# Performance work log

Hardware: AMD Instinct MI355X
Metric: run time of the kernel (lower is better)

The kernel has to match this reference:

```python
import jax, jax.numpy as jnp
import numpy as np

D_MODEL = 1024
NHEAD = 16
D_K = D_MODEL // NHEAD


def setup_inputs() -> dict:
    key = jax.random.key(0)
    ks = jax.random.split(key, 12)
    B, L = 4, 2048
    s = 1.0 / np.sqrt(D_MODEL)
    inp = {
        "query": jax.random.normal(ks[0], (B, L, D_MODEL), jnp.float32),
        "key": jax.random.normal(ks[1], (B, L, D_MODEL), jnp.float32),
        "value": jax.random.normal(ks[2], (B, L, D_MODEL), jnp.float32),
        "Wq": jax.random.normal(ks[3], (D_MODEL, D_MODEL), jnp.float32) * s,
        "bq": jnp.zeros((D_MODEL,), jnp.float32),
        "Wk": jax.random.normal(ks[4], (D_MODEL, D_MODEL), jnp.float32) * s,
        "bk": jnp.zeros((D_MODEL,), jnp.float32),
        "Wv": jax.random.normal(ks[5], (D_MODEL, D_MODEL), jnp.float32) * s,
        "bv": jnp.zeros((D_MODEL,), jnp.float32),
        "Wo": jax.random.normal(ks[6], (D_MODEL, D_MODEL), jnp.float32) * s,
        "bo": jnp.zeros((D_MODEL,), jnp.float32),
    }
    return inp


def reference(query, key, value, Wq, bq, Wk, bk, Wv, bv, Wo, bo):
    B, Lq, _ = query.shape
    Lk = key.shape[1]
    # Linear projections, split into heads: [B, H, L, d_k]
    Q = (query @ Wq + bq).reshape(B, Lq, NHEAD, D_K).transpose(0, 2, 1, 3)
    K = (key @ Wk + bk).reshape(B, Lk, NHEAD, D_K).transpose(0, 2, 1, 3)
    V = (value @ Wv + bv).reshape(B, Lk, NHEAD, D_K).transpose(0, 2, 1, 3)
    scale = 1.0 / jnp.sqrt(jnp.asarray(D_K, Q.dtype))
    scores = jnp.einsum("bhqd,bhkd->bhqk", Q, K) * scale  # [B,H,Lq,Lk]
    attn = jax.nn.softmax(scores, axis=-1)
    context = jnp.einsum("bhqk,bhkd->bhqd", attn, V)
    context = context.transpose(0, 2, 1, 3).reshape(B, Lq, D_MODEL)
    return context @ Wo + bo
```

## Files before the change

kernel.cpp:

```cpp
#include <hip/hip_runtime.h>
#include <hip/hip_bf16.h>
#include <cstdint>
#include <cstddef>


typedef unsigned short u16;
typedef __bf16 bf8v __attribute__((ext_vector_type(8)));
typedef __bf16 bf4v __attribute__((ext_vector_type(4)));
typedef float f32x4 __attribute__((ext_vector_type(4)));

#define D_MODEL 1024
#define NHEAD   16
#define DK      64
#define BATCH   4
#define SEQ     2048
#define ROWS    (BATCH * SEQ)

__device__ __forceinline__ u16 f2b(float f) {
  union { float f; unsigned int i; } x; x.f = f;
  unsigned int r = x.i + 0x7fffu + ((x.i >> 16) & 1u);
  return (u16)(r >> 16);
}
__device__ __forceinline__ ushort4 pack4(float a, float b, float c, float d) {
  union { bf4v v; ushort4 u; } x;
  x.v[0] = (__bf16)a; x.v[1] = (__bf16)b; x.v[2] = (__bf16)c; x.v[3] = (__bf16)d;
  return x.u;
}
__device__ __forceinline__ bf8v cvt8(float4 a, float4 b) {
  bf8v r;
  r[0] = (__bf16)a.x; r[1] = (__bf16)a.y; r[2] = (__bf16)a.z; r[3] = (__bf16)a.w;
  r[4] = (__bf16)b.x; r[5] = (__bf16)b.y; r[6] = (__bf16)b.z; r[7] = (__bf16)b.w;
  return r;
}
__device__ __forceinline__ void async16(const void* g, void* l) {
  __builtin_amdgcn_global_load_lds((const __attribute__((address_space(1))) void*)g,
                                   (__attribute__((address_space(3))) void*)l, 16, 0, 0);
}
#define MFMA16(a, b, c) __builtin_amdgcn_mfma_f32_16x16x32_bf16(a, b, c, 0, 0, 0)

__global__ void wtrans_cvt_kernel(const float* __restrict__ w0, const float* __restrict__ w1,
                                  const float* __restrict__ w2, const float* __restrict__ w3,
                                  u16* __restrict__ dst4) {
  __shared__ float t[32][33];
  const float* src = (blockIdx.z == 0) ? w0 : (blockIdx.z == 1) ? w1
                   : (blockIdx.z == 2) ? w2 : w3;
  u16* dst = dst4 + (size_t)blockIdx.z * D_MODEL * D_MODEL;
  const int c0 = blockIdx.x * 32, r0 = blockIdx.y * 32;
  for (int i = threadIdx.y; i < 32; i += 8)
    t[i][threadIdx.x] = src[(size_t)(r0 + i) * D_MODEL + c0 + threadIdx.x];
  __syncthreads();
  for (int i = threadIdx.y; i < 32; i += 8)
    dst[(size_t)(c0 + i) * D_MODEL + r0 + threadIdx.x] = f2b(t[threadIdx.x][i]);
}

#define BM 128
#define BN 128
#define BK 32

__global__ __launch_bounds__(256) void gemm_qkv(
    const float* __restrict__ Aq, const float* __restrict__ Ak,
    const float* __restrict__ Av, const u16* __restrict__ wt,
    const float* __restrict__ bq, const float* __restrict__ bk,
    const float* __restrict__ bv, u16* __restrict__ Qw, u16* __restrict__ Kw,
    u16* __restrict__ Vt, float qscale) {
  __shared__ __align__(16) u16 As[BM * BK];
  __shared__ __align__(16) u16 Bs[BN * BK];
  const int z = blockIdx.y;
  const float* A = (z == 0) ? Aq : (z == 1) ? Ak : Av;
  const u16* Bt = wt + (size_t)z * D_MODEL * D_MODEL;
  const float* bias = (z == 0) ? bq : (z == 1) ? bk : bv;
  u16* out = (z == 0) ? Qw : (z == 1) ? Kw : Vt;
  const float oscale = (z == 0) ? qscale : 1.0f;

  const int lid = blockIdx.x;
  const int xcd = lid & 7, jj = lid >> 3;
  const int m0 = ((xcd << 3) + (jj >> 3)) * BM;
  const int n0 = (jj & 7) * BN;

  const int tid = threadIdx.x;
  const int lane = tid & 63, wave = tid >> 6;
  const int wm = wave >> 1, wn = wave & 1;
  const int quad = lane >> 4, l16 = lane & 15;
  const int K = 1024;

  f32x4 acc[4][4];
#pragma unroll
  for (int i = 0; i < 4; i++)
#pragma unroll
    for (int j = 0; j < 4; j++) acc[i][j] = (f32x4){0.f, 0.f, 0.f, 0.f};

  const int srow = tid >> 2;
  const int sch = ((tid & 3) ^ ((tid >> 3) & 3)) * 8;
  const int fsw = (quad ^ ((l16 >> 1) & 3)) * 8;
  const float* Ag0 = A + (size_t)(m0 + srow) * K + sch;
  const float* Ag1 = Ag0 + (size_t)64 * K;
  const u16* Bg = Bt + (size_t)(n0 + srow) * K + sch;

  float4 ar0 = *(const float4*)(Ag0);
  float4 ar1 = *(const float4*)(Ag0 + 4);
  float4 ar2 = *(const float4*)(Ag1);
  float4 ar3 = *(const float4*)(Ag1 + 4);

  for (int k0 = 0; k0 < K; k0 += BK) {
    async16(Bg + k0, &Bs[tid * 8]);
    async16(Bg + (size_t)64 * K + k0, &Bs[2048 + tid * 8]);
    *(bf8v*)&As[tid * 8]        = cvt8(ar0, ar1);
    *(bf8v*)&As[2048 + tid * 8] = cvt8(ar2, ar3);
    __syncthreads();
    if (k0 + BK < K) {
      ar0 = *(const float4*)(Ag0 + k0 + BK);
      ar1 = *(const float4*)(Ag0 + k0 + BK + 4);
      ar2 = *(const float4*)(Ag1 + k0 + BK);
      ar3 = *(const float4*)(Ag1 + k0 + BK + 4);
    }

    bf8v af[4], bfr[4];
#pragma unroll
    for (int i = 0; i < 4; i++)
      af[i] = *(const bf8v*)&As[(wm * 64 + i * 16 + l16) * BK + fsw];
#pragma unroll
    for (int j = 0; j < 4; j++)
      bfr[j] = *(const bf8v*)&Bs[(wn * 64 + j * 16 + l16) * BK + fsw];
    if (z < 2) {
#pragma unroll
      for (int i = 0; i < 4; i++)
#pragma unroll
        for (int j = 0; j < 4; j++)
          acc[i][j] = MFMA16(bfr[j], af[i], acc[i][j]);
    } else {
#pragma unroll
      for (int i = 0; i < 4; i++)
#pragma unroll
        for (int j = 0; j < 4; j++)
          acc[i][j] = MFMA16(af[i], bfr[j], acc[i][j]);
    }
    __syncthreads();
  }

  if (z < 2) {
#pragma unroll
    for (int i = 0; i < 4; i++) {
      const int m = m0 + wm * 64 + i * 16 + l16;
      const int b = m >> 11, l = m & 2047;
#pragma unroll
      for (int j = 0; j < 4; j++) {
        const int n = n0 + wn * 64 + j * 16 + quad * 4;
        const float4 bv4 = *(const float4*)&bias[n];
        const int h = n >> 6, d = n & 63;
        *(ushort4*)&out[(((size_t)(b * NHEAD + h) * SEQ + l) << 6) + d] =
            pack4((acc[i][j][0] + bv4.x) * oscale, (acc[i][j][1] + bv4.y) * oscale,
                  (acc[i][j][2] + bv4.z) * oscale, (acc[i][j][3] + bv4.w) * oscale);
      }
    }
  } else {
#pragma unroll
    for (int j = 0; j < 4; j++) {
      const int n = n0 + wn * 64 + j * 16 + l16;
      const float bvs = bias[n];
      const int h = n >> 6, d = n & 63;
#pragma unroll
      for (int i = 0; i < 4; i++) {
        const int row = m0 + wm * 64 + i * 16 + quad * 4;
        const int b = row >> 11, l = row & 2047;
        const int pl = (l & ~31) | ((l & 12) << 1) | ((l & 16) >> 2);
        *(ushort4*)&out[(((size_t)(b * NHEAD + h) * DK + d) << 11) + pl] =
            pack4(acc[i][j][0] + bvs, acc[i][j][1] + bvs,
                  acc[i][j][2] + bvs, acc[i][j][3] + bvs);
      }
    }
  }
}

__global__ __launch_bounds__(256) void gemm_out(const u16* __restrict__ A,
                                                const u16* __restrict__ Bt,
                                                const float* __restrict__ bias,
                                                float* __restrict__ out) {
  __shared__ __align__(16) u16 As[BM * BK];
  __shared__ __align__(16) u16 Bs[BN * BK];
  const int lid = blockIdx.x;
  const int xcd = lid & 7, jj = lid >> 3;
  const int m0 = ((xcd << 3) + (jj >> 3)) * BM;
  const int n0 = (jj & 7) * BN;
  const int tid = threadIdx.x;
  const int lane = tid & 63, wave = tid >> 6;
  const int wm = wave >> 1, wn = wave & 1;
  const int quad = lane >> 4, l16 = lane & 15;
  const int K = 1024;

  f32x4 acc[4][4];
#pragma unroll
  for (int i = 0; i < 4; i++)
#pragma unroll
    for (int j = 0; j < 4; j++) acc[i][j] = (f32x4){0.f, 0.f, 0.f, 0.f};

  const int srow = tid >> 2;
  const int sch = ((tid & 3) ^ ((tid >> 3) & 3)) * 8;
  const int fsw = (quad ^ ((l16 >> 1) & 3)) * 8;
  const u16* Ag = A + (size_t)(m0 + srow) * K + sch;
  const u16* Bg = Bt + (size_t)(n0 + srow) * K + sch;

  for (int k0 = 0; k0 < K; k0 += BK) {
    async16(Ag + k0, &As[tid * 8]);
    async16(Ag + (size_t)64 * K + k0, &As[2048 + tid * 8]);
    async16(Bg + k0, &Bs[tid * 8]);
    async16(Bg + (size_t)64 * K + k0, &Bs[2048 + tid * 8]);
    __syncthreads();

    bf8v af[4], bfr[4];
#pragma unroll
    for (int i = 0; i < 4; i++)
      af[i] = *(const bf8v*)&As[(wm * 64 + i * 16 + l16) * BK + fsw];
#pragma unroll
    for (int j = 0; j < 4; j++)
      bfr[j] = *(const bf8v*)&Bs[(wn * 64 + j * 16 + l16) * BK + fsw];
#pragma unroll
    for (int i = 0; i < 4; i++)
#pragma unroll
      for (int j = 0; j < 4; j++)
        acc[i][j] = MFMA16(bfr[j], af[i], acc[i][j]);
    __syncthreads();
  }

#pragma unroll
  for (int i = 0; i < 4; i++) {
    const int m = m0 + wm * 64 + i * 16 + l16;
#pragma unroll
    for (int j = 0; j < 4; j++) {
      const int n = n0 + wn * 64 + j * 16 + quad * 4;
      const float4 bv4 = *(const float4*)&bias[n];
      float4 vv;
      vv.x = acc[i][j][0] + bv4.x; vv.y = acc[i][j][1] + bv4.y;
      vv.z = acc[i][j][2] + bv4.z; vv.w = acc[i][j][3] + bv4.w;
      *(float4*)&out[(size_t)m * D_MODEL + n] = vv;
    }
  }
}

__global__ __launch_bounds__(256, 4) void attn_kernel(const u16* __restrict__ Q,
                                                      const u16* __restrict__ K,
                                                      const u16* __restrict__ Vt,
                                                      u16* __restrict__ ctx) {
  const int bh = blockIdx.x;
  const int qb = blockIdx.y * 128;
  const int tid = threadIdx.x;
  const int lane = tid & 63, wave = tid >> 6;
  const int quad = lane >> 4, l16 = lane & 15;
  const u16* Qh = Q + (size_t)bh * SEQ * DK;
  const u16* Kh = K + (size_t)bh * SEQ * DK;
  const u16* Vh = Vt + (size_t)bh * DK * SEQ;

  __shared__ __align__(16) u16 Ks[2][2][64 * 32];
  __shared__ __align__(16) u16 Vs[2][64 * 64];

  const int srow = tid >> 2;
  const int sch  = ((tid & 3) ^ ((tid >> 3) & 3)) * 8;
  const int ldst = tid * 8;
  const int fsw  = (quad ^ ((l16 >> 1) & 3)) * 8;
  const int vd   = tid >> 3;
  const int vcol = ((tid & 7) ^ ((tid >> 3) & 7)) * 8;

  bf8v qf[2][2];
#pragma unroll
  for (int qg = 0; qg < 2; qg++)
#pragma unroll
    for (int h = 0; h < 2; h++)
      qf[qg][h] = *(const bf8v*)&Qh[(size_t)(qb + wave * 32 + qg * 16 + l16) * DK + h * 32 + quad * 8];

  bf8v ones;
#pragma unroll
  for (int j = 0; j < 8; j++) ones[j] = (__bf16)1.0f;

  f32x4 o[2][4];
  f32x4 la[2];
  float m_q[2];
#pragma unroll
  for (int qg = 0; qg < 2; qg++) {
    m_q[qg] = -1e30f; la[qg] = (f32x4){0.f, 0.f, 0.f, 0.f};
#pragma unroll
    for (int d = 0; d < 4; d++) o[qg][d] = (f32x4){0.f, 0.f, 0.f, 0.f};
  }

  async16(Kh + (size_t)srow * DK + sch,      &Ks[0][0][ldst]);
  async16(Kh + (size_t)srow * DK + 32 + sch, &Ks[0][1][ldst]);
  async16(Vh + (size_t)vd * SEQ + vcol,        &Vs[0][ldst]);
  async16(Vh + (size_t)(vd + 32) * SEQ + vcol, &Vs[0][2048 + ldst]);
  __syncthreads();

  int p = 0;
  for (int kt = 0; kt < SEQ; kt += 64) {
    const int nt = kt + 64;
    if (nt < SEQ) {
      async16(Kh + (size_t)(nt + srow) * DK + sch,      &Ks[p ^ 1][0][ldst]);
      async16(Kh + (size_t)(nt + srow) * DK + 32 + sch, &Ks[p ^ 1][1][ldst]);
      async16(Vh + (size_t)vd * SEQ + nt + vcol,        &Vs[p ^ 1][ldst]);
      async16(Vh + (size_t)(vd + 32) * SEQ + nt + vcol, &Vs[p ^ 1][2048 + ldst]);
    }

    bf8v kf[4][2];
#pragma unroll
    for (int nb = 0; nb < 4; nb++)
#pragma unroll
      for (int h = 0; h < 2; h++)
        kf[nb][h] = *(const bf8v*)&Ks[p][h][(nb * 16 + l16) * 32 + fsw];

    bf8v pf[2][2];
#pragma unroll
    for (int qg = 0; qg < 2; qg++) {
      f32x4 s[4];
      __builtin_amdgcn_s_setprio(1);
#pragma unroll
      for (int nb = 0; nb < 4; nb++) {
        f32x4 t = (f32x4){0.f, 0.f, 0.f, 0.f};
        t = MFMA16(kf[nb][0], qf[qg][0], t);
        t = MFMA16(kf[nb][1], qf[qg][1], t);
        s[nb] = t;
      }
      __builtin_amdgcn_s_setprio(0);
      float t0 = fmaxf(fmaxf(s[0][0], s[0][1]), fmaxf(s[0][2], s[0][3]));
      float t1 = fmaxf(fmaxf(s[1][0], s[1][1]), fmaxf(s[1][2], s[1][3]));
      float t2 = fmaxf(fmaxf(s[2][0], s[2][1]), fmaxf(s[2][2], s[2][3]));
      float t3 = fmaxf(fmaxf(s[3][0], s[3][1]), fmaxf(s[3][2], s[3][3]));
      float mx = fmaxf(fmaxf(t0, t1), fmaxf(t2, t3));
      mx = fmaxf(mx, __shfl_xor(mx, 16));
      mx = fmaxf(mx, __shfl_xor(mx, 32));
      const float mprev = m_q[qg];
      float Mn = mprev;
      const int resc = !__all(mx - mprev <= 8.0f);
      if (resc) {
        Mn = fmaxf(mprev, mx);
        const float al = __builtin_amdgcn_exp2f(mprev - Mn);
        m_q[qg] = Mn;
        la[qg] *= al;
#pragma unroll
        for (int d = 0; d < 4; d++) o[qg][d] *= al;
      }
#pragma unroll
      for (int nb = 0; nb < 4; nb++)
#pragma unroll
        for (int r = 0; r < 4; r++)
          s[nb][r] = __builtin_amdgcn_exp2f(s[nb][r] - Mn);
#pragma unroll
      for (int kc = 0; kc < 2; kc++) {
        bf8v pw;
#pragma unroll
        for (int j = 0; j < 4; j++) {
          pw[j]     = (__bf16)s[2 * kc][j];
          pw[j + 4] = (__bf16)s[2 * kc + 1][j];
        }
        pf[qg][kc] = pw;
      }
      la[qg] = MFMA16(ones, pf[qg][0], la[qg]);
      la[qg] = MFMA16(ones, pf[qg][1], la[qg]);
    }

    bf8v vf[4][2];
#pragma unroll
    for (int dc = 0; dc < 4; dc++) {
      const int rb = (dc * 16 + l16) * 64;
#pragma unroll
      for (int kc = 0; kc < 2; kc++)
        vf[dc][kc] = *(const bf8v*)&Vs[p][rb + (((kc * 4 + quad) ^ (l16 & 7)) * 8)];
    }
    __builtin_amdgcn_s_setprio(1);
#pragma unroll
    for (int qg = 0; qg < 2; qg++)
#pragma unroll
      for (int dc = 0; dc < 4; dc++) {
        o[qg][dc] = MFMA16(vf[dc][0], pf[qg][0], o[qg][dc]);
        o[qg][dc] = MFMA16(vf[dc][1], pf[qg][1], o[qg][dc]);
      }
    __builtin_amdgcn_s_setprio(0);

    __syncthreads();
    p ^= 1;
  }

  const int b = bh >> 4, hh = bh & 15;
#pragma unroll
  for (int qg = 0; qg < 2; qg++) {
    const float inv = __builtin_amdgcn_rcpf(la[qg][0]);
    const int q = qb + wave * 32 + qg * 16 + l16;
#pragma unroll
    for (int dc = 0; dc < 4; dc++) {
      const int col = hh * 64 + dc * 16 + quad * 4;
      *(ushort4*)&ctx[(size_t)(b * SEQ + q) * D_MODEL + col] =
          pack4(o[qg][dc][0] * inv, o[qg][dc][1] * inv,
                o[qg][dc][2] * inv, o[qg][dc][3] * inv);
    }
  }
}

extern "C" void kernel_launch(void* const* d_in, const int* in_sizes, int n_in,
                              void* d_out, int out_size, void* d_ws, size_t ws_size,
                              hipStream_t stream) {
  const float* q  = (const float*)d_in[0];
  const float* k  = (const float*)d_in[1];
  const float* v  = (const float*)d_in[2];
  const float* Wq = (const float*)d_in[3];
  const float* bq = (const float*)d_in[4];
  const float* Wk = (const float*)d_in[5];
  const float* bk = (const float*)d_in[6];
  const float* Wv = (const float*)d_in[7];
  const float* bv = (const float*)d_in[8];
  const float* Wo = (const float*)d_in[9];
  const float* bo = (const float*)d_in[10];

  u16* ws  = (u16*)d_ws;
  u16* wt  = ws;
  u16* Qw  = wt + (size_t)4 * D_MODEL * D_MODEL;
  u16* Kw  = Qw + (size_t)ROWS * D_MODEL;
  u16* Vt  = Kw + (size_t)ROWS * D_MODEL;
  u16* ctx = Vt + (size_t)ROWS * D_MODEL;

  const float QSCALE = 0.18033688011112042f;

  wtrans_cvt_kernel<<<dim3(32, 32, 4), dim3(32, 8), 0, stream>>>(Wq, Wk, Wv, Wo, wt);

  gemm_qkv<<<dim3(512, 3), 256, 0, stream>>>(q, k, v, wt, bq, bk, bv, Qw, Kw, Vt, QSCALE);

  attn_kernel<<<dim3(BATCH * NHEAD, SEQ / 128), 256, 0, stream>>>(Qw, Kw, Vt, ctx);

  gemm_out<<<512, 256, 0, stream>>>(ctx, wt + (size_t)3 * D_MODEL * D_MODEL, bo,
                                    (float*)d_out);
}
```

Baseline: 378.4 us.

## Double-buffer LDS tiles in QKV and output projection GEMMs

Both projection GEMMs now use two LDS buffers per operand. The next K-tile is written into the alternate buffer while MFMAs consume the current one, so each iteration needs one barrier instead of two and global load latency overlaps compute. This doubles LDS usage per block, and launch bounds now request two blocks per CU. Async copies into the alternate buffer may not be waited on explicitly before the barrier, depending on how async16 is implemented.

```diff
diff --git a/kernel.cpp b/kernel.cpp
--- a/kernel.cpp
+++ b/kernel.cpp
@@ -57,14 +57,14 @@
 #define BN 128
 #define BK 32
 
-__global__ __launch_bounds__(256) void gemm_qkv(
+__global__ __launch_bounds__(256, 2) void gemm_qkv(
     const float* __restrict__ Aq, const float* __restrict__ Ak,
     const float* __restrict__ Av, const u16* __restrict__ wt,
     const float* __restrict__ bq, const float* __restrict__ bk,
     const float* __restrict__ bv, u16* __restrict__ Qw, u16* __restrict__ Kw,
     u16* __restrict__ Vt, float qscale) {
-  __shared__ __align__(16) u16 As[BM * BK];
-  __shared__ __align__(16) u16 Bs[BN * BK];
+  __shared__ __align__(16) u16 As[2][BM * BK];
+  __shared__ __align__(16) u16 Bs[2][BN * BK];
   const int z = blockIdx.y;
   const float* A = (z == 0) ? Aq : (z == 1) ? Ak : Av;
   const u16* Bt = wt + (size_t)z * D_MODEL * D_MODEL;
@@ -96,31 +96,43 @@
   const float* Ag1 = Ag0 + (size_t)64 * K;
   const u16* Bg = Bt + (size_t)(n0 + srow) * K + sch;
 
-  float4 ar0 = *(const float4*)(Ag0);
-  float4 ar1 = *(const float4*)(Ag0 + 4);
-  float4 ar2 = *(const float4*)(Ag1);
-  float4 ar3 = *(const float4*)(Ag1 + 4);
-
+  float4 a0 = *(const float4*)(Ag0);
+  float4 a1 = *(const float4*)(Ag0 + 4);
+  float4 a2 = *(const float4*)(Ag1);
+  float4 a3 = *(const float4*)(Ag1 + 4);
+  async16(Bg, &Bs[0][tid * 8]);
+  async16(Bg + (size_t)64 * K, &Bs[0][2048 + tid * 8]);
+  *(bf8v*)&As[0][tid * 8]        = cvt8(a0, a1);
+  *(bf8v*)&As[0][2048 + tid * 8] = cvt8(a2, a3);
+  a0 = *(const float4*)(Ag0 + BK);
+  a1 = *(const float4*)(Ag0 + BK + 4);
+  a2 = *(const float4*)(Ag1 + BK);
+  a3 = *(const float4*)(Ag1 + BK + 4);
+  __syncthreads();
+
+  int p = 0;
   for (int k0 = 0; k0 < K; k0 += BK) {
-    async16(Bg + k0, &Bs[tid * 8]);
-    async16(Bg + (size_t)64 * K + k0, &Bs[2048 + tid * 8]);
-    *(bf8v*)&As[tid * 8]        = cvt8(ar0, ar1);
-    *(bf8v*)&As[2048 + tid * 8] = cvt8(ar2, ar3);
-    __syncthreads();
-    if (k0 + BK < K) {
-      ar0 = *(const float4*)(Ag0 + k0 + BK);
-      ar1 = *(const float4*)(Ag0 + k0 + BK + 4);
-      ar2 = *(const float4*)(Ag1 + k0 + BK);
-      ar3 = *(const float4*)(Ag1 + k0 + BK + 4);
+    const int kn = k0 + BK;
+    if (kn < K) {
+      async16(Bg + kn, &Bs[p ^ 1][tid * 8]);
+      async16(Bg + (size_t)64 * K + kn, &Bs[p ^ 1][2048 + tid * 8]);
+      *(bf8v*)&As[p ^ 1][tid * 8]        = cvt8(a0, a1);
+      *(bf8v*)&As[p ^ 1][2048 + tid * 8] = cvt8(a2, a3);
+      if (kn + BK < K) {
+        a0 = *(const float4*)(Ag0 + kn + BK);
+        a1 = *(const float4*)(Ag0 + kn + BK + 4);
+        a2 = *(const float4*)(Ag1 + kn + BK);
+        a3 = *(const float4*)(Ag1 + kn + BK + 4);
+      }
     }
 
     bf8v af[4], bfr[4];
 #pragma unroll
     for (int i = 0; i < 4; i++)
-      af[i] = *(const bf8v*)&As[(wm * 64 + i * 16 + l16) * BK + fsw];
+      af[i] = *(const bf8v*)&As[p][(wm * 64 + i * 16 + l16) * BK + fsw];
 #pragma unroll
     for (int j = 0; j < 4; j++)
-      bfr[j] = *(const bf8v*)&Bs[(wn * 64 + j * 16 + l16) * BK + fsw];
+      bfr[j] = *(const bf8v*)&Bs[p][(wn * 64 + j * 16 + l16) * BK + fsw];
     if (z < 2) {
 #pragma unroll
       for (int i = 0; i < 4; i++)
@@ -135,6 +147,7 @@
           acc[i][j] = MFMA16(af[i], bfr[j], acc[i][j]);
     }
     __syncthreads();
+    p ^= 1;
   }
 
   if (z < 2) {
@@ -171,12 +184,12 @@
   }
 }
 
-__global__ __launch_bounds__(256) void gemm_out(const u16* __restrict__ A,
-                                                const u16* __restrict__ Bt,
-                                                const float* __restrict__ bias,
-                                                float* __restrict__ out) {
-  __shared__ __align__(16) u16 As[BM * BK];
-  __shared__ __align__(16) u16 Bs[BN * BK];
+__global__ __launch_bounds__(256, 2) void gemm_out(const u16* __restrict__ A,
+                                                   const u16* __restrict__ Bt,
+                                                   const float* __restrict__ bias,
+                                                   float* __restrict__ out) {
+  __shared__ __align__(16) u16 As[2][BM * BK];
+  __shared__ __align__(16) u16 Bs[2][BN * BK];
   const int lid = blockIdx.x;
   const int xcd = lid & 7, jj = lid >> 3;
   const int m0 = ((xcd << 3) + (jj >> 3)) * BM;
@@ -199,26 +212,36 @@
   const u16* Ag = A + (size_t)(m0 + srow) * K + sch;
   const u16* Bg = Bt + (size_t)(n0 + srow) * K + sch;
 
+  async16(Ag, &As[0][tid * 8]);
+  async16(Ag + (size_t)64 * K, &As[0][2048 + tid * 8]);
+  async16(Bg, &Bs[0][tid * 8]);
+  async16(Bg + (size_t)64 * K, &Bs[0][2048 + tid * 8]);
+  __syncthreads();
+
+  int p = 0;
   for (int k0 = 0; k0 < K; k0 += BK) {
-    async16(Ag + k0, &As[tid * 8]);
-    async16(Ag + (size_t)64 * K + k0, &As[2048 + tid * 8]);
-    async16(Bg + k0, &Bs[tid * 8]);
-    async16(Bg + (size_t)64 * K + k0, &Bs[2048 + tid * 8]);
-    __syncthreads();
+    const int kn = k0 + BK;
+    if (kn < K) {
+      async16(Ag + kn, &As[p ^ 1][tid * 8]);
+      async16(Ag + (size_t)64 * K + kn, &As[p ^ 1][2048 + tid * 8]);
+      async16(Bg + kn, &Bs[p ^ 1][tid * 8]);
+      async16(Bg + (size_t)64 * K + kn, &Bs[p ^ 1][2048 + tid * 8]);
+    }
 
     bf8v af[4], bfr[4];
 #pragma unroll
     for (int i = 0; i < 4; i++)
-      af[i] = *(const bf8v*)&As[(wm * 64 + i * 16 + l16) * BK + fsw];
+      af[i] = *(const bf8v*)&As[p][(wm * 64 + i * 16 + l16) * BK + fsw];
 #pragma unroll
     for (int j = 0; j < 4; j++)
-      bfr[j] = *(const bf8v*)&Bs[(wn * 64 + j * 16 + l16) * BK + fsw];
+      bfr[j] = *(const bf8v*)&Bs[p][(wn * 64 + j * 16 + l16) * BK + fsw];
 #pragma unroll
     for (int i = 0; i < 4; i++)
 #pragma unroll
       for (int j = 0; j < 4; j++)
         acc[i][j] = MFMA16(bfr[j], af[i], acc[i][j]);
     __syncthreads();
+    p ^= 1;
   }
 
 #pragma unroll
```

Measured after the change: 384.0 us. About the same (+1.5%).
